# Optimization experiments

Measured on AMD Instinct MI355X. Metric: run time of the kernel, lower is better.

Reference implementation:

```python
import jax, jax.numpy as jnp
import numpy as np

H, DK, DV, DEMB = 16, 64, 64, 1024
D_MODEL = H * DV


def setup_inputs() -> dict:
    key = jax.random.key(0)
    ks = jax.random.split(key, 9)
    scale = 0.02
    x = jax.random.normal(ks[0], (4, 2048, DEMB), dtype=jnp.float32)
    wq = jax.random.normal(ks[1], (DEMB, H * DK), dtype=jnp.float32) * scale
    bq = jnp.zeros((H * DK,), dtype=jnp.float32)
    wk = jax.random.normal(ks[2], (DEMB, H * DK), dtype=jnp.float32) * scale
    bk = jnp.zeros((H * DK,), dtype=jnp.float32)
    wv = jax.random.normal(ks[3], (DEMB, H * DV), dtype=jnp.float32) * scale
    bv = jnp.zeros((H * DV,), dtype=jnp.float32)
    wo = jax.random.normal(ks[4], (D_MODEL, D_MODEL), dtype=jnp.float32) * scale
    bo = jnp.zeros((D_MODEL,), dtype=jnp.float32)
    return {"x": x, "wq": wq, "bq": bq, "wk": wk, "bk": bk,
            "wv": wv, "bv": bv, "wo": wo, "bo": bo, "mask": 0}


def _split_heads(t, h):
    # (b, s, h*d) -> (b, h, s, d)
    b, s, _ = t.shape
    return t.reshape(b, s, h, -1).transpose(0, 2, 1, 3)


def reference(x, wq, bq, wk, bk, wv, bv, wo, bo, mask):
    b, s, _ = x.shape
    qs = _split_heads(x @ wq + bq, H)  # (b, h, s, dk)
    ks = _split_heads(x @ wk + bk, H)
    vs = _split_heads(x @ wv + bv, H)  # (b, h, s, dv)
    # FAITHFUL quirk: original scales by 1/sqrt(len(ks[0])) == 1/sqrt(n_heads),
    # not 1/sqrt(d_k).
    scores = jnp.einsum('bhqd,bhkd->bhqk', qs, ks) / jnp.sqrt(jnp.float32(H))
    # FAITHFUL quirk: masked_fill(mask == 0, ...) with scalar bool mask is a
    # no-op (True == 0 is False), so no masking is ever applied.
    attn = jax.nn.softmax(scores, axis=-1)
    out = jnp.einsum('bhqk,bhkd->bhqd', attn, vs)  # (b, h, s, dv)
    out = out.transpose(0, 2, 1, 3).reshape(b, s, D_MODEL)
    return out @ wo + bo
```

## Files before the change

### kernel.cpp

```cpp
#include <hip/hip_runtime.h>
#include <stdint.h>

typedef __attribute__((ext_vector_type(8))) short short8;
typedef __attribute__((ext_vector_type(4))) short short4v;
typedef __attribute__((ext_vector_type(4))) float floatx4;
typedef __attribute__((ext_vector_type(4))) _Float16 half4;
typedef __attribute__((ext_vector_type(2))) __fp16 pk2;

#define SEQ 2048
#define NTOK 8192
#define QSCALE 0.360673760222241f

#define MFMA16F16(a,b,c) __builtin_amdgcn_mfma_f32_16x16x16f16((a),(b),(c),0,0,0)

__device__ __forceinline__ float b2f(unsigned short u){
  union { unsigned int i; float f; } v; v.i = ((unsigned int)u) << 16; return v.f;
}
__device__ __forceinline__ unsigned short f2b(float f){
  union { float f; unsigned int i; } v; v.f = f;
  unsigned int r = v.i + 0x7fffu + ((v.i >> 16) & 1u);
  return (unsigned short)(r >> 16);
}
__device__ __forceinline__ void async16(const unsigned short* g, unsigned short* l){
  __builtin_amdgcn_global_load_lds(
      (const __attribute__((address_space(1))) unsigned int*)g,
      (__attribute__((address_space(3))) unsigned int*)l, 16, 0, 0);
}

__global__ __launch_bounds__(256) void prep_kernel(
    const float* __restrict__ x,
    const float* __restrict__ wq, const float* __restrict__ wk,
    const float* __restrict__ wv, const float* __restrict__ wo,
    const float* __restrict__ bq, const float* __restrict__ bk,
    const float* __restrict__ bv,
    unsigned short* __restrict__ xb,
    unsigned short* __restrict__ wqkvT, unsigned short* __restrict__ woT,
    float* __restrict__ bqkv)
{
  __shared__ unsigned short lT[64][72];
  const int bid = blockIdx.x;
  const int tid = threadIdx.x;
  if (bid < 8192){
    int i = (bid*256 + tid)*4;
    float4 v = *(const float4*)(x + i);
    short4v o;
    o[0] = (short)f2b(v.x); o[1] = (short)f2b(v.y);
    o[2] = (short)f2b(v.z); o[3] = (short)f2b(v.w);
    *(short4v*)(xb + i) = o;
  } else if (bid < 9216){
    int idx = bid - 8192;
    int sel = idx >> 8, rest = idx & 255;
    const float* src = (sel==0)?wq:(sel==1)?wk:(sel==2)?wv:wo;
    unsigned short* dst = (sel<3) ? (wqkvT + (size_t)sel*1024*1024) : woT;
    int n0 = (rest & 15) * 64, k0 = (rest >> 4) * 64;
#pragma unroll
    for (int i=0;i<4;i++){
      int ch = tid + i*256;
      int r = ch>>4, c = (ch&15)*4;
      float4 v = *(const float4*)(src + (size_t)(k0+r)*1024 + n0 + c);
      lT[r][c+0] = f2b(v.x); lT[r][c+1] = f2b(v.y);
      lT[r][c+2] = f2b(v.z); lT[r][c+3] = f2b(v.w);
    }
    __syncthreads();
#pragma unroll
    for (int i=0;i<2;i++){
      int ch = tid + i*256;
      int rn = ch>>3, c = (ch&7)*8;
      short8 v;
#pragma unroll
      for (int j=0;j<8;j++) v[j] = (short)lT[c+j][rn];
      *(short8*)(dst + (size_t)(n0+rn)*1024 + k0 + c) = v;
    }
  } else {
    int i = (bid - 9216)*256 + tid;
    if (i < 3072){
      int sel = i >> 10, j = i & 1023;
      bqkv[i] = (sel==0)?bq[j]:(sel==1)?bk[j]:bv[j];
    }
  }
}

template<int OUT_F32, int SCALE_Q>
__global__ __launch_bounds__(256) void gemm_bt_kernel(
    const unsigned short* __restrict__ A,
    const unsigned short* __restrict__ Bt,
    const float* __restrict__ bias,
    void* __restrict__ Cv,
    int M, int N, int K)
{
  __shared__ unsigned short lA[128*64];
  __shared__ unsigned short lB[128*64];
  const int tid  = threadIdx.x;
  const int lane = tid & 63;
  const int wave = tid >> 6;
  const int quad = lane >> 4;
  const int l15  = lane & 15;
  const int wR = (wave >> 1) * 64;
  const int wC = (wave & 1) * 64;
  const int rowB = blockIdx.y * 128;
  const int colB = blockIdx.x * 128;

  const int srow = wave*32 + (lane>>3);
  const int sc8  = (lane&7) ^ (lane>>3);
  const unsigned short* gA = A  + (size_t)(rowB + srow)*K + sc8*8;
  const unsigned short* gB = Bt + (size_t)(colB + srow)*K + sc8*8;
  unsigned short* lAw = lA + wave*32*64 + lane*8;
  unsigned short* lBw = lB + wave*32*64 + lane*8;

  floatx4 acc[4][4];
#pragma unroll
  for (int t=0;t<4;t++)
#pragma unroll
    for (int u=0;u<4;u++) acc[t][u] = (floatx4){0.f,0.f,0.f,0.f};

  for (int kt = 0; kt < K; kt += 64){
    __syncthreads();
#pragma unroll
    for (int i=0;i<4;i++){
      async16(gA + (size_t)i*8*K + kt, lAw + i*512);
      async16(gB + (size_t)i*8*K + kt, lBw + i*512);
    }
    __syncthreads();
#pragma unroll
    for (int ks=0; ks<2; ks++){
      const int cph = ((ks*4 + quad) ^ (l15 & 7)) * 8;
      short8 af[4], bf[4];
#pragma unroll
      for (int t=0;t<4;t++) af[t] = *(const short8*)&lA[(wR + t*16 + l15)*64 + cph];
#pragma unroll
      for (int u=0;u<4;u++) bf[u] = *(const short8*)&lB[(wC + u*16 + l15)*64 + cph];
#pragma unroll
      for (int t=0;t<4;t++)
#pragma unroll
        for (int u=0;u<4;u++)
          acc[t][u] = __builtin_amdgcn_mfma_f32_16x16x32_bf16(af[t], bf[u], acc[t][u], 0, 0, 0);
    }
  }
#pragma unroll
  for (int u=0;u<4;u++){
    int col = colB + wC + u*16 + l15;
    float bval = bias[col];
    float scale = (SCALE_Q && col < 1024) ? QSCALE : 1.0f;
#pragma unroll
    for (int t=0;t<4;t++){
      int row0 = rowB + wR + t*16 + quad*4;
#pragma unroll
      for (int r=0;r<4;r++){
        float val = (acc[t][u][r] + bval) * scale;
        if (OUT_F32) ((float*)Cv)[(size_t)(row0 + r)*N + col] = val;
        else ((unsigned short*)Cv)[(size_t)(row0 + r)*N + col] = f2b(val);
      }
    }
  }
}

__global__ __launch_bounds__(256) void transpose_v_kernel(
    const unsigned short* __restrict__ qkv,
    unsigned short* __restrict__ vt)
{
  __shared__ unsigned short lT[64][72];
  const int bh = blockIdx.x;
  const int b = bh >> 4, h = bh & 15;
  const int s0 = blockIdx.y * 64;
  const int tid = threadIdx.x;
#pragma unroll
  for (int i=0;i<2;i++){
    int ch = tid + i*256;
    int r = ch >> 3, c = (ch & 7)*8;
    short8 raw = *(const short8*)(qkv + (size_t)(b*SEQ + s0 + r)*3072 + 2048 + h*64 + c);
#pragma unroll
    for (int j=0;j<8;j++){
      union { _Float16 h; unsigned short u; } cv;
      cv.h = (_Float16)b2f((unsigned short)raw[j]);
      lT[r][c+j] = cv.u;
    }
  }
  __syncthreads();
#pragma unroll
  for (int i=0;i<2;i++){
    int ch = tid + i*256;
    int dv = ch >> 3, c = (ch & 7)*8;
    short8 v;
#pragma unroll
    for (int j=0;j<8;j++) v[j] = (short)lT[c+j][dv];
    *(short8*)(vt + (size_t)(bh*64 + dv)*2048 + s0 + c) = v;
  }
}

__global__ __launch_bounds__(256) void flash_attn_kernel(
    const unsigned short* __restrict__ qkv,
    const unsigned short* __restrict__ vt,
    unsigned short* __restrict__ attn_out)
{
  __shared__ unsigned short sK[2][64*64];
  __shared__ _Float16 sV[2][64*64];
  const int bh = blockIdx.x;
  const int b = bh >> 4, h = bh & 15;
  const int qt = blockIdx.y;
  const int tid = threadIdx.x;
  const int wave = tid >> 6;
  const int lane = tid & 63;
  const int quad = lane >> 4, l15 = lane & 15;
  const int tok0 = b*SEQ + qt*128;

  const int srow = lane >> 3;
  const int sc8  = (lane & 7) ^ srow;
  const unsigned short* gK = qkv + (size_t)(b*SEQ + wave*16 + srow)*3072 + 1024 + h*64 + sc8*8;
  const unsigned short* gV = vt  + (size_t)(bh*64 + wave*16 + srow)*2048 + sc8*8;
  const int ldso = (wave*16)*64 + lane*8;

  short8 qf[2][2];
#pragma unroll
  for (int t=0;t<2;t++)
#pragma unroll
    for (int ks=0;ks<2;ks++)
      qf[t][ks] = *(const short8*)(qkv + (size_t)(tok0 + wave*32 + t*16 + l15)*3072
                                   + h*64 + ks*32 + quad*8);

  floatx4 oacc[2][4];
  float psum[2] = {0.f, 0.f};
#pragma unroll
  for (int t=0;t<2;t++)
#pragma unroll
    for (int v=0;v<4;v++) oacc[t][v] = (floatx4){0.f,0.f,0.f,0.f};

#pragma unroll
  for (int i=0;i<2;i++){
    async16(gK + (size_t)i*8*3072, &sK[0][ldso + i*512]);
    async16(gV + (size_t)i*8*2048, (unsigned short*)&sV[0][ldso + i*512]);
  }
  __syncthreads();

  for (int it = 0; it < SEQ/64; it++){
    const int bi = it & 1;
    if (it + 1 < SEQ/64){
      const int nx = (it + 1) * 64;
#pragma unroll
      for (int i=0;i<2;i++){
        async16(gK + (size_t)(i*8 + (size_t)nx)*3072, &sK[bi^1][ldso + i*512]);
        async16(gV + (size_t)i*8*2048 + nx, (unsigned short*)&sV[bi^1][ldso + i*512]);
      }
    }

    floatx4 sacc[4][2];
#pragma unroll
    for (int u=0;u<4;u++)
#pragma unroll
      for (int t=0;t<2;t++) sacc[u][t] = (floatx4){0.f,0.f,0.f,0.f};
#pragma unroll
    for (int ks=0;ks<2;ks++){
      const int cph = ((ks*4 + quad) ^ (l15 & 7)) * 8;
      short8 kf[4];
#pragma unroll
      for (int u=0;u<4;u++) kf[u] = *(const short8*)&sK[bi][(u*16 + l15)*64 + cph];
#pragma unroll
      for (int u=0;u<4;u++)
#pragma unroll
        for (int t=0;t<2;t++)
          sacc[u][t] = __builtin_amdgcn_mfma_f32_16x16x32_bf16(kf[u], qf[t][ks], sacc[u][t], 0,0,0);
    }

    half4 pf[4][2];
#pragma unroll
    for (int t=0;t<2;t++){
#pragma unroll
      for (int u=0;u<4;u++){
        float p0 = __builtin_amdgcn_exp2f(sacc[u][t][0]);
        float p1 = __builtin_amdgcn_exp2f(sacc[u][t][1]);
        float p2 = __builtin_amdgcn_exp2f(sacc[u][t][2]);
        float p3 = __builtin_amdgcn_exp2f(sacc[u][t][3]);
        psum[t] += (p0+p1)+(p2+p3);
        union { pk2 p2v[2]; half4 h4; } cv;
        cv.p2v[0] = __builtin_amdgcn_cvt_pkrtz(p0,p1);
        cv.p2v[1] = __builtin_amdgcn_cvt_pkrtz(p2,p3);
        pf[u][t] = cv.h4;
      }
    }

#pragma unroll
    for (int v=0;v<4;v++){
      half4 vf[4];
#pragma unroll
      for (int u=0;u<4;u++){
        const int cph = ((2*u + (quad>>1)) ^ (l15 & 7)) * 8 + (quad&1)*4;
        vf[u] = *(const half4*)&sV[bi][(v*16 + l15)*64 + cph];
      }
#pragma unroll
      for (int t=0;t<2;t++)
#pragma unroll
        for (int u=0;u<4;u++)
          oacc[t][v] = MFMA16F16(pf[u][t], vf[u], oacc[t][v]);
    }
    __syncthreads();
  }

#pragma unroll
  for (int t=0;t<2;t++){
    float s = psum[t];
    s += __shfl_xor(s, 16);
    s += __shfl_xor(s, 32);
    psum[t] = s;
  }
#pragma unroll
  for (int t=0;t<2;t++){
#pragma unroll
    for (int r=0;r<4;r++){
      float inv = 1.0f / __shfl(psum[t], quad*4 + r);
      int tok = tok0 + wave*32 + t*16 + quad*4 + r;
#pragma unroll
      for (int v=0;v<4;v++)
        attn_out[(size_t)tok*1024 + h*64 + v*16 + l15] = f2b(oacc[t][v][r] * inv);
    }
  }
}

extern "C" void kernel_launch(void* const* d_in, const int* in_sizes, int n_in,
                              void* d_out, int out_size, void* d_ws, size_t ws_size,
                              hipStream_t stream)
{
  const float* x  = (const float*)d_in[0];
  const float* wq = (const float*)d_in[1];
  const float* bq = (const float*)d_in[2];
  const float* wk = (const float*)d_in[3];
  const float* bk = (const float*)d_in[4];
  const float* wv = (const float*)d_in[5];
  const float* bv = (const float*)d_in[6];
  const float* wo = (const float*)d_in[7];
  const float* bo = (const float*)d_in[8];
  float* out = (float*)d_out;

  char* ws = (char*)d_ws;
  unsigned short* wqkvT  = (unsigned short*)(ws);
  unsigned short* woT    = (unsigned short*)(ws + 6291456);
  float*          bqkv   = (float*)(ws + 8388608);
  unsigned short* xb     = (unsigned short*)(ws + 8400896);
  unsigned short* qkvbuf = (unsigned short*)(ws + 25178112);
  unsigned short* vtbuf  = (unsigned short*)(ws + 75509760);
  unsigned short* aobuf  = (unsigned short*)(ws + 92286976);

  prep_kernel<<<dim3(9228), 256, 0, stream>>>(x, wq, wk, wv, wo, bq, bk, bv,
                                              xb, wqkvT, woT, bqkv);
  gemm_bt_kernel<0,1><<<dim3(24, 64), 256, 0, stream>>>(xb, wqkvT, bqkv, qkvbuf, 8192, 3072, 1024);
  transpose_v_kernel<<<dim3(64, 32), 256, 0, stream>>>(qkvbuf, vtbuf);
  flash_attn_kernel<<<dim3(64, 16), 256, 0, stream>>>(qkvbuf, vtbuf, aobuf);
  gemm_bt_kernel<1,0><<<dim3(8, 64), 256, 0, stream>>>(aobuf, woT, bo, out, 8192, 1024, 1024);
}
```

Baseline: 314.9 us.

## Fuse V transpose into QKV GEMM epilogue and restage attention K/V loads

```diff
diff --git a/kernel.cpp b/kernel.cpp
--- a/kernel.cpp
+++ b/kernel.cpp
@@ -80,12 +80,13 @@
   }
 }
 
-template<int OUT_F32, int SCALE_Q>
+template<int MODE>
 __global__ __launch_bounds__(256) void gemm_bt_kernel(
     const unsigned short* __restrict__ A,
     const unsigned short* __restrict__ Bt,
     const float* __restrict__ bias,
     void* __restrict__ Cv,
+    unsigned short* __restrict__ Vt,
     int M, int N, int K)
 {
   __shared__ unsigned short lA[128*64];
@@ -136,54 +137,40 @@
           acc[t][u] = __builtin_amdgcn_mfma_f32_16x16x32_bf16(af[t], bf[u], acc[t][u], 0, 0, 0);
     }
   }
-#pragma unroll
-  for (int u=0;u<4;u++){
-    int col = colB + wC + u*16 + l15;
-    float bval = bias[col];
-    float scale = (SCALE_Q && col < 1024) ? QSCALE : 1.0f;
-#pragma unroll
-    for (int t=0;t<4;t++){
-      int row0 = rowB + wR + t*16 + quad*4;
-#pragma unroll
-      for (int r=0;r<4;r++){
-        float val = (acc[t][u][r] + bval) * scale;
-        if (OUT_F32) ((float*)Cv)[(size_t)(row0 + r)*N + col] = val;
-        else ((unsigned short*)Cv)[(size_t)(row0 + r)*N + col] = f2b(val);
-      }
-    }
-  }
-}
-
-__global__ __launch_bounds__(256) void transpose_v_kernel(
-    const unsigned short* __restrict__ qkv,
-    unsigned short* __restrict__ vt)
-{
-  __shared__ unsigned short lT[64][72];
-  const int bh = blockIdx.x;
-  const int b = bh >> 4, h = bh & 15;
-  const int s0 = blockIdx.y * 64;
-  const int tid = threadIdx.x;
-#pragma unroll
-  for (int i=0;i<2;i++){
-    int ch = tid + i*256;
-    int r = ch >> 3, c = (ch & 7)*8;
-    short8 raw = *(const short8*)(qkv + (size_t)(b*SEQ + s0 + r)*3072 + 2048 + h*64 + c);
-#pragma unroll
-    for (int j=0;j<8;j++){
-      union { _Float16 h; unsigned short u; } cv;
-      cv.h = (_Float16)b2f((unsigned short)raw[j]);
-      lT[r][c+j] = cv.u;
-    }
-  }
-  __syncthreads();
-#pragma unroll
-  for (int i=0;i<2;i++){
-    int ch = tid + i*256;
-    int dv = ch >> 3, c = (ch & 7)*8;
-    short8 v;
-#pragma unroll
-    for (int j=0;j<8;j++) v[j] = (short)lT[c+j][dv];
-    *(short8*)(vt + (size_t)(bh*64 + dv)*2048 + s0 + c) = v;
+  if (MODE == 3 && colB >= 2048){
+#pragma unroll
+    for (int u=0;u<4;u++){
+      int col = colB + wC + u*16 + l15;
+      float bval = bias[col];
+      int vcol = col - 2048;
+      int hh = vcol >> 6, dv = vcol & 63;
+#pragma unroll
+      for (int t=0;t<4;t++){
+        int row0 = rowB + wR + t*16 + quad*4;
+        int bb = row0 >> 11, s = row0 & 2047;
+        union { pk2 p[2]; short4v s4; } cv;
+        cv.p[0] = __builtin_amdgcn_cvt_pkrtz(acc[t][u][0]+bval, acc[t][u][1]+bval);
+        cv.p[1] = __builtin_amdgcn_cvt_pkrtz(acc[t][u][2]+bval, acc[t][u][3]+bval);
+        *(short4v*)(Vt + ((size_t)(bb*16+hh)*64 + dv)*2048 + s) = cv.s4;
+      }
+    }
+  } else {
+#pragma unroll
+    for (int u=0;u<4;u++){
+      int col = colB + wC + u*16 + l15;
+      float bval = bias[col];
+      float scale = (MODE == 3 && col < 1024) ? QSCALE : 1.0f;
+#pragma unroll
+      for (int t=0;t<4;t++){
+        int row0 = rowB + wR + t*16 + quad*4;
+#pragma unroll
+        for (int r=0;r<4;r++){
+          float val = (acc[t][u][r] + bval) * scale;
+          if (MODE == 1) ((float*)Cv)[(size_t)(row0 + r)*N + col] = val;
+          else ((unsigned short*)Cv)[(size_t)(row0 + r)*N + col] = f2b(val);
+        }
+      }
+    }
   }
 }
 
@@ -192,8 +179,8 @@
     const unsigned short* __restrict__ vt,
     unsigned short* __restrict__ attn_out)
 {
-  __shared__ unsigned short sK[2][64*64];
-  __shared__ _Float16 sV[2][64*64];
+  __shared__ unsigned short sK[2][64][72];
+  __shared__ unsigned short sVt[2][64][72];
   const int bh = blockIdx.x;
   const int b = bh >> 4, h = bh & 15;
   const int qt = blockIdx.y;
@@ -203,12 +190,6 @@
   const int quad = lane >> 4, l15 = lane & 15;
   const int tok0 = b*SEQ + qt*128;
 
-  const int srow = lane >> 3;
-  const int sc8  = (lane & 7) ^ srow;
-  const unsigned short* gK = qkv + (size_t)(b*SEQ + wave*16 + srow)*3072 + 1024 + h*64 + sc8*8;
-  const unsigned short* gV = vt  + (size_t)(bh*64 + wave*16 + srow)*2048 + sc8*8;
-  const int ldso = (wave*16)*64 + lane*8;
-
   short8 qf[2][2];
 #pragma unroll
   for (int t=0;t<2;t++)
@@ -224,74 +205,95 @@
 #pragma unroll
     for (int v=0;v<4;v++) oacc[t][v] = (floatx4){0.f,0.f,0.f,0.f};
 
-#pragma unroll
-  for (int i=0;i<2;i++){
-    async16(gK + (size_t)i*8*3072, &sK[0][ldso + i*512]);
-    async16(gV + (size_t)i*8*2048, (unsigned short*)&sV[0][ldso + i*512]);
-  }
-  __syncthreads();
-
-  for (int it = 0; it < SEQ/64; it++){
-    const int bi = it & 1;
-    if (it + 1 < SEQ/64){
-      const int nx = (it + 1) * 64;
-#pragma unroll
-      for (int i=0;i<2;i++){
-        async16(gK + (size_t)(i*8 + (size_t)nx)*3072, &sK[bi^1][ldso + i*512]);
-        async16(gV + (size_t)i*8*2048 + nx, (unsigned short*)&sV[bi^1][ldso + i*512]);
-      }
-    }
-
-    floatx4 sacc[4][2];
-#pragma unroll
-    for (int u=0;u<4;u++)
-#pragma unroll
-      for (int t=0;t<2;t++) sacc[u][t] = (floatx4){0.f,0.f,0.f,0.f};
-#pragma unroll
-    for (int ks=0;ks<2;ks++){
-      const int cph = ((ks*4 + quad) ^ (l15 & 7)) * 8;
-      short8 kf[4];
-#pragma unroll
-      for (int u=0;u<4;u++) kf[u] = *(const short8*)&sK[bi][(u*16 + l15)*64 + cph];
+  int R[4], C[4], HF[4], U[4], QD[4];
+#pragma unroll
+  for (int i=0;i<4;i++){
+    int chh = tid + (i&1)*256;
+    R[i] = chh >> 3; C[i] = (chh & 7)*8; HF[i] = i >> 1;
+    U[i] = C[i] >> 4; QD[i] = (C[i] & 15) >> 2;
+  }
+  short8 rk[4], rv[4];
+#pragma unroll
+  for (int i=0;i<4;i++){
+    rk[i] = *(const short8*)(qkv + (size_t)(b*SEQ + HF[i]*64 + R[i])*3072 + 1024 + h*64 + C[i]);
+    rv[i] = *(const short8*)(vt  + (size_t)(bh*64 + R[i])*2048 + HF[i]*64 + C[i]);
+  }
+
+  for (int it = 0; it < SEQ/128; it++){
+    __syncthreads();
+#pragma unroll
+    for (int i=0;i<4;i++){
+      *(short8*)&sK[HF[i]][R[i]][C[i]] = rk[i];
+      short4v lo = {rv[i][0],rv[i][1],rv[i][2],rv[i][3]};
+      short4v hi = {rv[i][4],rv[i][5],rv[i][6],rv[i][7]};
+      *(short4v*)&sVt[HF[i]][R[i]][QD[i]*16 + U[i]*4]     = lo;
+      *(short4v*)&sVt[HF[i]][R[i]][(QD[i]+1)*16 + U[i]*4] = hi;
+    }
+    __syncthreads();
+    if (it + 1 < SEQ/128){
+      int nx = (it + 1) * 128;
+#pragma unroll
+      for (int i=0;i<4;i++){
+        rk[i] = *(const short8*)(qkv + (size_t)(b*SEQ + nx + HF[i]*64 + R[i])*3072 + 1024 + h*64 + C[i]);
+        rv[i] = *(const short8*)(vt  + (size_t)(bh*64 + R[i])*2048 + nx + HF[i]*64 + C[i]);
+      }
+    }
+
+#pragma unroll
+    for (int hf=0; hf<2; hf++){
+      floatx4 sacc[4][2];
 #pragma unroll
       for (int u=0;u<4;u++)
 #pragma unroll
+        for (int t=0;t<2;t++) sacc[u][t] = (floatx4){0.f,0.f,0.f,0.f};
+#pragma unroll
+      for (int ks=0;ks<2;ks++){
+        short8 kf[4];
+#pragma unroll
+        for (int u=0;u<4;u++) kf[u] = *(const short8*)&sK[hf][u*16 + l15][ks*32 + quad*8];
+#pragma unroll
+        for (int u=0;u<4;u++)
+#pragma unroll
+          for (int t=0;t<2;t++)
+            sacc[u][t] = __builtin_amdgcn_mfma_f32_16x16x32_bf16(kf[u], qf[t][ks], sacc[u][t], 0,0,0);
+      }
+
+      half4 pf[4][2];
+#pragma unroll
+      for (int t=0;t<2;t++){
+#pragma unroll
+        for (int u=0;u<4;u++){
+          float p0 = __builtin_amdgcn_exp2f(sacc[u][t][0]);
+          float p1 = __builtin_amdgcn_exp2f(sacc[u][t][1]);
+          float p2 = __builtin_amdgcn_exp2f(sacc[u][t][2]);
+          float p3 = __builtin_amdgcn_exp2f(sacc[u][t][3]);
+          psum[t] += (p0+p1)+(p2+p3);
+          union { pk2 p2v[2]; half4 h4; } cv;
+          cv.p2v[0] = __builtin_amdgcn_cvt_pkrtz(p0,p1);
+          cv.p2v[1] = __builtin_amdgcn_cvt_pkrtz(p2,p3);
+          pf[u][t] = cv.h4;
+        }
+      }
+
+#pragma unroll
+      for (int v=0;v<4;v++){
+        half4 vf[4];
+#pragma unroll
+        for (int hh=0;hh<2;hh++){
+          short8 w = *(const short8*)&sVt[hf][v*16 + l15][quad*16 + hh*8];
+          union { short4v s; half4 h; } a, bb;
+          a.s  = (short4v){w[0],w[1],w[2],w[3]};
+          bb.s = (short4v){w[4],w[5],w[6],w[7]};
+          vf[2*hh]   = a.h;
+          vf[2*hh+1] = bb.h;
+        }
+#pragma unroll
         for (int t=0;t<2;t++)
-          sacc[u][t] = __builtin_amdgcn_mfma_f32_16x16x32_bf16(kf[u], qf[t][ks], sacc[u][t], 0,0,0);
-    }
-
-    half4 pf[4][2];
-#pragma unroll
-    for (int t=0;t<2;t++){
-#pragma unroll
-      for (int u=0;u<4;u++){
-        float p0 = __builtin_amdgcn_exp2f(sacc[u][t][0]);
-        float p1 = __builtin_amdgcn_exp2f(sacc[u][t][1]);
-        float p2 = __builtin_amdgcn_exp2f(sacc[u][t][2]);
-        float p3 = __builtin_amdgcn_exp2f(sacc[u][t][3]);
-        psum[t] += (p0+p1)+(p2+p3);
-        union { pk2 p2v[2]; half4 h4; } cv;
-        cv.p2v[0] = __builtin_amdgcn_cvt_pkrtz(p0,p1);
-        cv.p2v[1] = __builtin_amdgcn_cvt_pkrtz(p2,p3);
-        pf[u][t] = cv.h4;
-      }
-    }
-
-#pragma unroll
-    for (int v=0;v<4;v++){
-      half4 vf[4];
-#pragma unroll
-      for (int u=0;u<4;u++){
-        const int cph = ((2*u + (quad>>1)) ^ (l15 & 7)) * 8 + (quad&1)*4;
-        vf[u] = *(const half4*)&sV[bi][(v*16 + l15)*64 + cph];
-      }
-#pragma unroll
-      for (int t=0;t<2;t++)
-#pragma unroll
-        for (int u=0;u<4;u++)
-          oacc[t][v] = MFMA16F16(pf[u][t], vf[u], oacc[t][v]);
-    }
-    __syncthreads();
+#pragma unroll
+          for (int u=0;u<4;u++)
+            oacc[t][v] = MFMA16F16(pf[u][t], vf[u], oacc[t][v]);
+      }
+    }
   }
 
 #pragma unroll
@@ -340,8 +342,9 @@
 
   prep_kernel<<<dim3(9228), 256, 0, stream>>>(x, wq, wk, wv, wo, bq, bk, bv,
                                               xb, wqkvT, woT, bqkv);
-  gemm_bt_kernel<0,1><<<dim3(24, 64), 256, 0, stream>>>(xb, wqkvT, bqkv, qkvbuf, 8192, 3072, 1024);
-  transpose_v_kernel<<<dim3(64, 32), 256, 0, stream>>>(qkvbuf, vtbuf);
+  gemm_bt_kernel<3><<<dim3(24, 64), 256, 0, stream>>>(xb, wqkvT, bqkv, qkvbuf, vtbuf,
+                                                      8192, 3072, 1024);
   flash_attn_kernel<<<dim3(64, 16), 256, 0, stream>>>(qkvbuf, vtbuf, aobuf);
-  gemm_bt_kernel<1,0><<<dim3(8, 64), 256, 0, stream>>>(aobuf, woT, bo, out, 8192, 1024, 1024);
-}
+  gemm_bt_kernel<1><<<dim3(8, 64), 256, 0, stream>>>(aobuf, woT, bo, out, nullptr,
+                                                     8192, 1024, 1024);
+}
```

Result: faster. 292.4 us (-7.1%).
